# Performance work log

Measured on AMD Instinct MI355X. Metric: run time of the kernel, lower is better.

The kernel has to match this reference:

```python
import jax, jax.numpy as jnp
import numpy as np
from jax import lax

SPATIAL = 4
DN = ('NCHW', 'OIHW', 'NCHW')

def setup_inputs() -> dict:
    key = jax.random.key(0)
    ks = jax.random.split(key, 6)
    b, c_in, h, w = 32, 256, 56, 56
    c_out, kk, n_exp, red = 256, 3, 3, 16
    fan = c_in * kk * kk
    return {
        'x': jax.random.normal(ks[0], (b, c_in, h, w), jnp.float32),
        'w_expert': jax.random.normal(ks[1], (n_exp, c_out, c_in, kk, kk), jnp.float32) / np.sqrt(fan),
        'route_conv_w': jax.random.normal(ks[2], (red, c_in), jnp.float32) / np.sqrt(c_in),
        'route_conv_b': jax.random.normal(ks[3], (red,), jnp.float32) * 0.05,
        'fc_w': jax.random.normal(ks[4], (n_exp, red * SPATIAL * SPATIAL), jnp.float32) / np.sqrt(red * SPATIAL * SPATIAL),
        'fc_b': jax.random.normal(ks[5], (n_exp,), jnp.float32) * 0.05,
    }

def _routing(x, route_conv_w, route_conv_b, fc_w, fc_b):
    b, c, h, w = x.shape
    # AdaptiveAvgPool2d(4): h, w divisible by 4 -> exact block mean
    pooled = x.reshape(b, c, SPATIAL, h // SPATIAL, SPATIAL, w // SPATIAL).mean(axis=(3, 5))  # [b,c,4,4]
    r = jnp.einsum('bcij,rc->brij', pooled, route_conv_w) + route_conv_b[None, :, None, None]
    r = jax.nn.relu(r).reshape(b, -1)                         # [b, red*16]
    r = jax.nn.relu(r @ fc_w.T + fc_b)                        # [b, n_exp]
    return jax.nn.sigmoid(r)

def reference(x, w_expert, route_conv_w, route_conv_b, fc_w, fc_b):
    rw = _routing(x, route_conv_w, route_conv_b, fc_w, fc_b)              # [b,k]
    cw = jnp.einsum('bk,koihw->boihw', rw, w_expert)                      # per-sample mixed weights
    def conv1(xi, wi):
        return lax.conv_general_dilated(xi[None], wi, window_strides=(1, 1),
                                        padding=[(1, 1), (1, 1)],
                                        dimension_numbers=DN)[0]
    return jax.vmap(conv1)(x, cw)  # [b, c_out, h, w]
```

## Files before the change

### kernel.cpp

```cpp
#include <hip/hip_runtime.h>
#include <hip/hip_bf16.h>
#include <stdint.h>

#define NB   32
#define CIN  256
#define COUT 256
#define WW   56
#define HW   3136
#define NEXP 3
#define KTOT 2304
#define XP   58
#define XPP  3364
#define NKT  36

typedef __attribute__((ext_vector_type(8))) __bf16 bf16x8;
typedef __attribute__((ext_vector_type(4))) float  f32x4;

#define OFF_RW     0
#define OFF_POOLED 1024
#define OFF_CWT    (1024 + 32*256*16*4)
#define CWT_BYTES  ((size_t)NB*COUT*KTOT*2)
#define OFF_XPAD   (OFF_CWT + CWT_BYTES)

__global__ __launch_bounds__(256) void k_pool(const float* __restrict__ x,
                                              float* __restrict__ pooled) {
    int b = blockIdx.x, c = blockIdx.y;
    const float* xb = x + ((size_t)(b * CIN + c)) * HW;
    __shared__ float lds[4][56];
    int t = threadIdx.x;
    if (t < 224) {
        int xc = t % 56, yg = t / 56;
        const float* p = xb + (yg * 14) * WW + xc;
        float s = 0.f;
        #pragma unroll
        for (int r = 0; r < 14; ++r) s += p[r * WW];
        lds[yg][xc] = s;
    }
    __syncthreads();
    if (t < 16) {
        int sy = t >> 2, sx = t & 3;
        float s = 0.f;
        #pragma unroll
        for (int j = 0; j < 14; ++j) s += lds[sy][sx * 14 + j];
        pooled[(((size_t)b * CIN + c) << 4) + t] = s * (1.f / 196.f);
    }
}

__global__ __launch_bounds__(256) void k_route(const float* __restrict__ pooled,
                                               const float* __restrict__ rcw,
                                               const float* __restrict__ rcb,
                                               const float* __restrict__ fcw,
                                               const float* __restrict__ fcb,
                                               float* __restrict__ rw) {
    int b = blockIdx.x;
    int t = threadIdx.x;
    int r = t >> 4, ij = t & 15;
    __shared__ float rbuf[256];
    const float* pb = pooled + (size_t)b * CIN * 16;
    float acc = rcb[r];
    for (int c = 0; c < CIN; ++c)
        acc += pb[c * 16 + ij] * rcw[r * CIN + c];
    rbuf[t] = fmaxf(acc, 0.f);
    __syncthreads();
    if (t < NEXP) {
        float a = fcb[t];
        for (int f = 0; f < 256; ++f) a += rbuf[f] * fcw[t * 256 + f];
        a = fmaxf(a, 0.f);
        rw[b * NEXP + t] = 1.f / (1.f + expf(-a));
    }
}

__global__ __launch_bounds__(256) void k_mixw(const float* __restrict__ we,
                                              const float* __restrict__ rw,
                                              __bf16* __restrict__ cwt) {
    int o = blockIdx.x;
    int i = threadIdx.x;
    float wv[3][9];
    #pragma unroll
    for (int e = 0; e < 3; ++e) {
        const float* p = we + (((size_t)e * COUT + o) * CIN + i) * 9;
        #pragma unroll
        for (int k = 0; k < 9; ++k) wv[e][k] = p[k];
    }
    for (int b = 0; b < NB; ++b) {
        float r0 = rw[b * 3 + 0], r1 = rw[b * 3 + 1], r2 = rw[b * 3 + 2];
        __bf16* op = cwt + ((size_t)(b * COUT + o)) * KTOT + i;
        #pragma unroll
        for (int k = 0; k < 9; ++k) {
            float v = r0 * wv[0][k] + r1 * wv[1][k] + r2 * wv[2][k];
            op[k * 256] = (__bf16)v;
        }
    }
}

__global__ __launch_bounds__(256) void k_zborder(__bf16* __restrict__ xpad) {
    int b = blockIdx.x;
    for (int idx = threadIdx.x; idx < 228 * 32; idx += 256) {
        int pos = idx >> 5;
        int co = (idx & 31) * 8;
        int yy, xx;
        if (pos < 58)       { yy = 0;          xx = pos; }
        else if (pos < 116) { yy = 57;         xx = pos - 58; }
        else if (pos < 172) { yy = pos - 115;  xx = 0; }
        else                { yy = pos - 171;  xx = 57; }
        uint4 z = {0u, 0u, 0u, 0u};
        *(uint4*)(xpad + ((size_t)b * XPP + yy * XP + xx) * CIN + co) = z;
    }
}

__global__ __launch_bounds__(256) void k_xpad(const float* __restrict__ x,
                                              __bf16* __restrict__ xpad) {
    int pt = blockIdx.x, ct = blockIdx.y, b = blockIdx.z;
    int t = threadIdx.x;
    __shared__ __bf16 lds[64][66];
    int pl = t & 63;
    int cb = t >> 6;
    const float* xb = x + ((size_t)(b * CIN + ct * 64)) * HW + pt * 64;
    #pragma unroll
    for (int ic = 0; ic < 16; ++ic) {
        int cl = ic * 4 + cb;
        lds[cl][pl] = (__bf16)xb[(size_t)cl * HW + pl];
    }
    __syncthreads();
    #pragma unroll
    for (int iw = 0; iw < 2; ++iw) {
        int idx = iw * 256 + t;
        int p_l = idx >> 3, c8 = (idx & 7) * 8;
        int p = pt * 64 + p_l;
        int y = p / WW, xx = p - y * WW;
        union { __bf16 h[8]; uint4 u; } pk;
        #pragma unroll
        for (int j = 0; j < 8; ++j) pk.h[j] = lds[c8 + j][p_l];
        __bf16* dst = xpad + ((size_t)b * XPP + (y + 1) * XP + (xx + 1)) * CIN
                      + ct * 64 + c8;
        *(uint4*)dst = pk.u;
    }
}

#define GL16(g, l) __builtin_amdgcn_global_load_lds( \
    (const __attribute__((address_space(1))) uint32_t*)(g), \
    (__attribute__((address_space(3))) uint32_t*)(l), 16, 0, 0)


#define STAGE_A(o, kh, aoffn) do { \
    GL16(gA0 + (aoffn) + (kh)*64, LDS + (o)*32768 + (kh)*16384 + wid*1024); \
    GL16(gA1 + (aoffn) + (kh)*64, LDS + (o)*32768 + (kh)*16384 + 8192 + wid*1024); \
  } while (0)
#define STAGE_B(o, kh, boffn) do { \
    GL16(gB0 + (boffn) + (kh)*64, LDS + 65536 + (o)*32768 + (kh)*16384 + wid*1024); \
    GL16(gB1 + (boffn) + (kh)*64, LDS + 65536 + (o)*32768 + (kh)*16384 + 8192 + wid*1024); \
  } while (0)

#define BARRIER() do { \
    __builtin_amdgcn_sched_barrier(0); \
    __builtin_amdgcn_s_barrier(); \
    __builtin_amdgcn_sched_barrier(0); \
  } while (0)

#define LOADA(aCur, kh, q) do { \
    af[0] = *(const bf16x8*)((aCur) + (kh)*16384 + (q)*4096 + 0); \
    af[1] = *(const bf16x8*)((aCur) + (kh)*16384 + (q)*4096 + 1024); \
    af[2] = *(const bf16x8*)((aCur) + (kh)*16384 + (q)*4096 + 2048); \
    af[3] = *(const bf16x8*)((aCur) + (kh)*16384 + (q)*4096 + 3072); \
  } while (0)
#define LOADB(bCur, kh) do { \
    bq[0] = *(const bf16x8*)((bCur) + (kh)*16384 + 0); \
    bq[1] = *(const bf16x8*)((bCur) + (kh)*16384 + 1024); \
    bq[2] = *(const bf16x8*)((bCur) + (kh)*16384 + 2048); \
    bq[3] = *(const bf16x8*)((bCur) + (kh)*16384 + 3072); \
  } while (0)
#define LGKM0() do { \
    asm volatile("s_waitcnt lgkmcnt(0)" ::: "memory"); \
    __builtin_amdgcn_sched_barrier(0); \
  } while (0)
#define MM(qb) do { \
    __builtin_amdgcn_s_setprio(1); \
    _Pragma("unroll") \
    for (int mf = 0; mf < 4; ++mf) \
      _Pragma("unroll") \
      for (int nf = 0; nf < 4; ++nf) \
        acc[(qb) + mf][nf] = __builtin_amdgcn_mfma_f32_16x16x32_bf16( \
            af[mf], bq[nf], acc[(qb) + mf][nf], 0, 0, 0); \
    __builtin_amdgcn_s_setprio(0); \
  } while (0)

__global__ __launch_bounds__(512, 2) void k_conv(const __bf16* __restrict__ cwt,
                                                 const __bf16* __restrict__ xpad,
                                                 float* __restrict__ out) {
    extern __shared__ __align__(16) char LDS[];

    int flat = blockIdx.x;
    int logical = (flat & 7) * 52 + (flat >> 3);
    int b  = logical / 13;
    int nt = logical - b * 13;

    int tid = threadIdx.x;
    int ln  = tid & 63;
    int wid = tid >> 6;
    int wr  = wid >> 2;
    int wc  = wid & 3;
    int fr  = ln & 15;
    int kw  = ln >> 4;
    int xsw = ((fr >> 1) & 3) << 4;

    const char *gA0, *gA1, *gB0, *gB1;
    {
        const char* cwb = (const char*)(cwt + (size_t)b * COUT * KTOT);
        const char* xpb = (const char*)(xpad + (size_t)b * XPP * CIN);
        #pragma unroll
        for (int i = 0; i < 2; ++i) {
            int L = i * 8192 + wid * 1024 + ln * 16;
            int U = L ^ (((L >> 7) & 3) << 4);
            int rowU = U >> 6;
            int kbU  = U & 63;
            const char* ga = cwb + (size_t)rowU * (KTOT * 2) + kbU;
            int p = nt * 256 + rowU; if (p > HW - 1) p = HW - 1;
            int y = p / WW, x = p - y * WW;
            const char* gb = xpb + (size_t)(y * XP + x) * (CIN * 2) + kbU;
            if (i == 0) { gA0 = ga; gB0 = gb; } else { gA1 = ga; gB1 = gb; }
        }
    }

    int aRd = (wr * 128 + fr) * 64 + ((kw * 16) ^ xsw);
    int bRd = (wc * 64 + fr) * 64 + ((kw * 16) ^ xsw);

    f32x4 acc[8][4];
    #pragma unroll
    for (int i = 0; i < 8; ++i)
        #pragma unroll
        for (int j = 0; j < 4; ++j)
            acc[i][j] = (f32x4){0.f, 0.f, 0.f, 0.f};

    bf16x8 af[4], bq[4];

    STAGE_A(0, 0, 0);
    STAGE_B(0, 0, 0);
    STAGE_A(0, 1, 0);
    STAGE_B(0, 1, 0);

    for (int kt = 0; kt < NKT - 1; ++kt) {
        int c = kt & 1, o = c ^ 1;
        int ktn  = kt + 1;
        int aoffn = ktn * 128;
        int ktap = ktn >> 2;
        int kyn  = (ktap * 11) >> 5;
        int kxn  = ktap - kyn * 3;
        int boffn = (kyn * XP + kxn) * 512 + (ktn & 3) * 128;
        const char* aCur = LDS + c * 32768 + aRd;
        const char* bCur = LDS + 65536 + c * 32768 + bRd;

        STAGE_A(o, 0, aoffn);
        asm volatile("s_waitcnt vmcnt(6)" ::: "memory");
        BARRIER();
        LOADA(aCur, 0, 0);
        LOADB(bCur, 0);
        LGKM0();
        MM(0);
        STAGE_B(o, 0, boffn);
        BARRIER();
        LOADA(aCur, 0, 1);
        LGKM0();
        MM(4);
        STAGE_A(o, 1, aoffn);
        asm volatile("s_waitcnt vmcnt(6)" ::: "memory");
        BARRIER();
        LOADA(aCur, 1, 0);
        LOADB(bCur, 1);
        LGKM0();
        MM(0);
        STAGE_B(o, 1, boffn);
        BARRIER();
        LOADA(aCur, 1, 1);
        LGKM0();
        MM(4);
    }

    {
        asm volatile("s_waitcnt vmcnt(0)" ::: "memory");
        BARRIER();
        const char* aCur = LDS + 32768 + aRd;
        const char* bCur = LDS + 65536 + 32768 + bRd;
        LOADA(aCur, 0, 0); LOADB(bCur, 0); LGKM0(); MM(0);
        LOADA(aCur, 0, 1);                 LGKM0(); MM(4);
        LOADA(aCur, 1, 0); LOADB(bCur, 1); LGKM0(); MM(0);
        LOADA(aCur, 1, 1);                 LGKM0(); MM(4);
    }

    float* ob = out + ((size_t)(b * COUT + wr * 128)) * HW;
    int colbase = nt * 256 + wc * 64;
    int rb = (ln >> 4) * 4;
    #pragma unroll
    for (int q = 0; q < 2; ++q)
        #pragma unroll
        for (int nf = 0; nf < 4; ++nf) {
            int col = colbase + nf * 16 + fr;
            if (col < HW) {
                #pragma unroll
                for (int mf = 0; mf < 4; ++mf)
                    #pragma unroll
                    for (int r = 0; r < 4; ++r)
                        ob[(size_t)(q * 64 + mf * 16 + rb + r) * HW + col] =
                            acc[q * 4 + mf][nf][r];
            }
        }
}

extern "C" void kernel_launch(void* const* d_in, const int* in_sizes, int n_in,
                              void* d_out, int out_size, void* d_ws, size_t ws_size,
                              hipStream_t stream) {
    (void)in_sizes; (void)n_in; (void)out_size; (void)ws_size;
    const float* x   = (const float*)d_in[0];
    const float* we  = (const float*)d_in[1];
    const float* rcw = (const float*)d_in[2];
    const float* rcb = (const float*)d_in[3];
    const float* fcw = (const float*)d_in[4];
    const float* fcb = (const float*)d_in[5];
    float* out = (float*)d_out;

    char* ws = (char*)d_ws;
    float*  rw     = (float*)(ws + OFF_RW);
    float*  pooled = (float*)(ws + OFF_POOLED);
    __bf16* cwt    = (__bf16*)(ws + OFF_CWT);
    __bf16* xpad   = (__bf16*)(ws + OFF_XPAD);

    (void)hipFuncSetAttribute((const void*)k_conv,
                              hipFuncAttributeMaxDynamicSharedMemorySize, 131072);

    k_zborder<<<NB, 256, 0, stream>>>(xpad);
    k_pool<<<dim3(NB, CIN), 256, 0, stream>>>(x, pooled);
    k_route<<<NB, 256, 0, stream>>>(pooled, rcw, rcb, fcw, fcb, rw);
    k_mixw<<<COUT, 256, 0, stream>>>(we, rw, cwt);
    k_xpad<<<dim3(49, 4, NB), 256, 0, stream>>>(x, xpad);
    k_conv<<<416, 512, 131072, stream>>>(cwt, xpad, out);
}
```

Measured before the change: 202.7 us.

## Fuse preprocessing kernels and cut conv main-loop barriers with deeper prefetch

The zero-border, pooling and bf16 padded-transpose kernels are merged into a single launch whose block index selects the role, saving two kernel launches and their serialisation gaps. In the conv GEMM main loop, the global-to-LDS staging for the next tile is now issued after the LDS fragment reads rather than before the barrier. The wait counts are tightened to vmcnt(4), which lets the loop drop two of its four barriers per K-tile. The reordering relies on exact per-thread vmcnt accounting to keep the double buffers race-free, so any change to the number of loads per stage would break it.

New measurement: 196.8 us. 1.03x faster.

```diff
diff --git a/kernel.cpp b/kernel.cpp
--- a/kernel.cpp
+++ b/kernel.cpp
@@ -22,27 +22,79 @@
 #define CWT_BYTES  ((size_t)NB*COUT*KTOT*2)
 #define OFF_XPAD   (OFF_CWT + CWT_BYTES)
 
-__global__ __launch_bounds__(256) void k_pool(const float* __restrict__ x,
-                                              float* __restrict__ pooled) {
-    int b = blockIdx.x, c = blockIdx.y;
-    const float* xb = x + ((size_t)(b * CIN + c)) * HW;
-    __shared__ float lds[4][56];
+#define PRE_XPAD 6272
+#define PRE_POOL 8192
+#define PRE_NBLK (PRE_XPAD + PRE_POOL + NB)
+
+__global__ __launch_bounds__(256) void k_pre(const float* __restrict__ x,
+                                             float* __restrict__ pooled,
+                                             __bf16* __restrict__ xpad) {
+    __shared__ __align__(16) char smem[8448];
+    int blk = blockIdx.x;
     int t = threadIdx.x;
-    if (t < 224) {
-        int xc = t % 56, yg = t / 56;
-        const float* p = xb + (yg * 14) * WW + xc;
-        float s = 0.f;
-        #pragma unroll
-        for (int r = 0; r < 14; ++r) s += p[r * WW];
-        lds[yg][xc] = s;
-    }
-    __syncthreads();
-    if (t < 16) {
-        int sy = t >> 2, sx = t & 3;
-        float s = 0.f;
-        #pragma unroll
-        for (int j = 0; j < 14; ++j) s += lds[sy][sx * 14 + j];
-        pooled[(((size_t)b * CIN + c) << 4) + t] = s * (1.f / 196.f);
+
+    if (blk < PRE_XPAD) {
+        int pt = blk % 49;
+        int r2 = blk / 49;
+        int ct = r2 & 3;
+        int b  = r2 >> 2;
+        __bf16 (*lds)[66] = (__bf16(*)[66])smem;
+        int pl = t & 63;
+        int cb = t >> 6;
+        const float* xb = x + ((size_t)(b * CIN + ct * 64)) * HW + pt * 64;
+        #pragma unroll
+        for (int ic = 0; ic < 16; ++ic) {
+            int cl = ic * 4 + cb;
+            lds[cl][pl] = (__bf16)xb[(size_t)cl * HW + pl];
+        }
+        __syncthreads();
+        #pragma unroll
+        for (int iw = 0; iw < 2; ++iw) {
+            int idx = iw * 256 + t;
+            int p_l = idx >> 3, c8 = (idx & 7) * 8;
+            int p = pt * 64 + p_l;
+            int y = p / WW, xx = p - y * WW;
+            union { __bf16 h[8]; uint4 u; } pk;
+            #pragma unroll
+            for (int j = 0; j < 8; ++j) pk.h[j] = lds[c8 + j][p_l];
+            __bf16* dst = xpad + ((size_t)b * XPP + (y + 1) * XP + (xx + 1)) * CIN
+                          + ct * 64 + c8;
+            *(uint4*)dst = pk.u;
+        }
+    } else if (blk < PRE_XPAD + PRE_POOL) {
+        int j = blk - PRE_XPAD;
+        int b = j >> 8, c = j & 255;
+        float (*lds)[56] = (float(*)[56])smem;
+        const float* xb = x + ((size_t)(b * CIN + c)) * HW;
+        if (t < 224) {
+            int xc = t % 56, yg = t / 56;
+            const float* p = xb + (yg * 14) * WW + xc;
+            float s = 0.f;
+            #pragma unroll
+            for (int r = 0; r < 14; ++r) s += p[r * WW];
+            lds[yg][xc] = s;
+        }
+        __syncthreads();
+        if (t < 16) {
+            int sy = t >> 2, sx = t & 3;
+            float s = 0.f;
+            #pragma unroll
+            for (int jj = 0; jj < 14; ++jj) s += lds[sy][sx * 14 + jj];
+            pooled[(((size_t)b * CIN + c) << 4) + t] = s * (1.f / 196.f);
+        }
+    } else {
+        int b = blk - (PRE_XPAD + PRE_POOL);
+        for (int idx = t; idx < 228 * 32; idx += 256) {
+            int pos = idx >> 5;
+            int co = (idx & 31) * 8;
+            int yy, xx;
+            if (pos < 58)       { yy = 0;          xx = pos; }
+            else if (pos < 116) { yy = 57;         xx = pos - 58; }
+            else if (pos < 172) { yy = pos - 115;  xx = 0; }
+            else                { yy = pos - 171;  xx = 57; }
+            uint4 z = {0u, 0u, 0u, 0u};
+            *(uint4*)(xpad + ((size_t)b * XPP + yy * XP + xx) * CIN + co) = z;
+        }
     }
 }
 
@@ -93,55 +145,10 @@
     }
 }
 
-__global__ __launch_bounds__(256) void k_zborder(__bf16* __restrict__ xpad) {
-    int b = blockIdx.x;
-    for (int idx = threadIdx.x; idx < 228 * 32; idx += 256) {
-        int pos = idx >> 5;
-        int co = (idx & 31) * 8;
-        int yy, xx;
-        if (pos < 58)       { yy = 0;          xx = pos; }
-        else if (pos < 116) { yy = 57;         xx = pos - 58; }
-        else if (pos < 172) { yy = pos - 115;  xx = 0; }
-        else                { yy = pos - 171;  xx = 57; }
-        uint4 z = {0u, 0u, 0u, 0u};
-        *(uint4*)(xpad + ((size_t)b * XPP + yy * XP + xx) * CIN + co) = z;
-    }
-}
-
-__global__ __launch_bounds__(256) void k_xpad(const float* __restrict__ x,
-                                              __bf16* __restrict__ xpad) {
-    int pt = blockIdx.x, ct = blockIdx.y, b = blockIdx.z;
-    int t = threadIdx.x;
-    __shared__ __bf16 lds[64][66];
-    int pl = t & 63;
-    int cb = t >> 6;
-    const float* xb = x + ((size_t)(b * CIN + ct * 64)) * HW + pt * 64;
-    #pragma unroll
-    for (int ic = 0; ic < 16; ++ic) {
-        int cl = ic * 4 + cb;
-        lds[cl][pl] = (__bf16)xb[(size_t)cl * HW + pl];
-    }
-    __syncthreads();
-    #pragma unroll
-    for (int iw = 0; iw < 2; ++iw) {
-        int idx = iw * 256 + t;
-        int p_l = idx >> 3, c8 = (idx & 7) * 8;
-        int p = pt * 64 + p_l;
-        int y = p / WW, xx = p - y * WW;
-        union { __bf16 h[8]; uint4 u; } pk;
-        #pragma unroll
-        for (int j = 0; j < 8; ++j) pk.h[j] = lds[c8 + j][p_l];
-        __bf16* dst = xpad + ((size_t)b * XPP + (y + 1) * XP + (xx + 1)) * CIN
-                      + ct * 64 + c8;
-        *(uint4*)dst = pk.u;
-    }
-}
-
 #define GL16(g, l) __builtin_amdgcn_global_load_lds( \
     (const __attribute__((address_space(1))) uint32_t*)(g), \
     (__attribute__((address_space(3))) uint32_t*)(l), 16, 0, 0)
 
-
 #define STAGE_A(o, kh, aoffn) do { \
     GL16(gA0 + (aoffn) + (kh)*64, LDS + (o)*32768 + (kh)*16384 + wid*1024); \
     GL16(gA1 + (aoffn) + (kh)*64, LDS + (o)*32768 + (kh)*16384 + 8192 + wid*1024); \
@@ -154,6 +161,10 @@
 #define BARRIER() do { \
     __builtin_amdgcn_sched_barrier(0); \
     __builtin_amdgcn_s_barrier(); \
+    __builtin_amdgcn_sched_barrier(0); \
+  } while (0)
+#define VMCNT(n) do { \
+    asm volatile("s_waitcnt vmcnt(" #n ")" ::: "memory"); \
     __builtin_amdgcn_sched_barrier(0); \
   } while (0)
 
@@ -249,34 +260,32 @@
         const char* aCur = LDS + c * 32768 + aRd;
         const char* bCur = LDS + 65536 + c * 32768 + bRd;
 
-        STAGE_A(o, 0, aoffn);
-        asm volatile("s_waitcnt vmcnt(6)" ::: "memory");
+        VMCNT(4);
         BARRIER();
         LOADA(aCur, 0, 0);
         LOADB(bCur, 0);
+        STAGE_A(o, 0, aoffn);
         LGKM0();
         MM(0);
+        LOADA(aCur, 0, 1);
         STAGE_B(o, 0, boffn);
-        BARRIER();
-        LOADA(aCur, 0, 1);
         LGKM0();
         MM(4);
-        STAGE_A(o, 1, aoffn);
-        asm volatile("s_waitcnt vmcnt(6)" ::: "memory");
+        VMCNT(4);
         BARRIER();
         LOADA(aCur, 1, 0);
         LOADB(bCur, 1);
+        STAGE_A(o, 1, aoffn);
         LGKM0();
         MM(0);
+        LOADA(aCur, 1, 1);
         STAGE_B(o, 1, boffn);
-        BARRIER();
-        LOADA(aCur, 1, 1);
         LGKM0();
         MM(4);
     }
 
     {
-        asm volatile("s_waitcnt vmcnt(0)" ::: "memory");
+        VMCNT(0);
         BARRIER();
         const char* aCur = LDS + 32768 + aRd;
         const char* bCur = LDS + 65536 + 32768 + bRd;
@@ -326,10 +335,8 @@
     (void)hipFuncSetAttribute((const void*)k_conv,
                               hipFuncAttributeMaxDynamicSharedMemorySize, 131072);
 
-    k_zborder<<<NB, 256, 0, stream>>>(xpad);
-    k_pool<<<dim3(NB, CIN), 256, 0, stream>>>(x, pooled);
+    k_pre<<<PRE_NBLK, 256, 0, stream>>>(x, pooled, xpad);
     k_route<<<NB, 256, 0, stream>>>(pooled, rcw, rcb, fcw, fcb, rw);
     k_mixw<<<COUT, 256, 0, stream>>>(we, rw, cwt);
-    k_xpad<<<dim3(49, 4, NB), 256, 0, stream>>>(x, xpad);
     k_conv<<<416, 512, 131072, stream>>>(cwt, xpad, out);
 }
```
